# Optimization experiments

Measured on AMD Instinct MI355X. Metric: run time of the kernel, lower is better.

## Reference

```python
import jax, jax.numpy as jnp
import numpy as np

N, F, H, O, D = 4096, 128, 4, 64, 64


def setup_inputs() -> dict:
    key = jax.random.key(0)
    k1, k2, k3, k4, k5 = jax.random.split(key, 5)
    h = jax.random.normal(k1, (1, N, F), dtype=jnp.float32)
    # dense binary adjacency (0/1)
    a = jax.random.randint(k2, (1, N, N), 0, 2).astype(jnp.float32)
    kernel = jax.random.normal(k3, (H, F, O), dtype=jnp.float32) * 0.1
    attn_kernel = jax.random.normal(k4, (H, F, D), dtype=jnp.float32) * 0.1
    attn_kernel2 = jax.random.normal(k5, (H, F, D), dtype=jnp.float32) * 0.1
    return {"h": h, "a": a, "kernel": kernel, "attn_kernel": attn_kernel, "attn_kernel2": attn_kernel2}


def reference(h, a, kernel, attn_kernel, attn_kernel2):
    x = h[0]          # [N, F]
    adj = a[0]        # [N, N] dense 0/1 adjacency
    # per-head linear projections, vectorized over heads
    feats = jnp.einsum('nf,hfo->hno', x, kernel)          # [H, N, O]
    f_self = jnp.einsum('nf,hfd->hnd', x, attn_kernel)    # [H, N, D]
    f_other = jnp.einsum('nf,hfd->hnd', x, attn_kernel2)  # [H, N, D]
    # dense attention logits, masked BEFORE the nonlinearity (as in original)
    dense = jnp.einsum('hnd,hmd->hnm', f_self, f_other)   # [H, N, N]
    masked = adj[None] * dense
    masked = jnp.where(masked >= 0, masked, 0.2 * masked)  # LeakyReLU(0.2)
    masked = masked / jnp.sqrt(jnp.asarray(D, jnp.float32))
    neg_inf = jnp.where(adj == 0, jnp.float32(-1e9), jnp.float32(0.0))  # [N, N]
    att = jax.nn.softmax(masked + neg_inf[None], axis=-1)
    att = att * (adj != 0).astype(att.dtype)[None]
    # aggregation (dropout is identity at inference, rate=0)
    node_features = jnp.einsum('hnm,hmo->hno', att, feats)  # [H, N, O]
    node_features = jax.nn.relu(node_features)
    # zero out padding rows (all-zero input features)
    row_mask = (jnp.sum((x != 0).astype(jnp.float32), axis=-1, keepdims=True) > 0).astype(jnp.float32)  # [N, 1]
    node_features = node_features * row_mask[None]
    # concat heads along last dim -> [1, N, H*O]
    out = jnp.transpose(node_features, (1, 0, 2)).reshape(N, H * O)
    return out[None]
```

## Files before the change

### kernel.cpp

```cpp
#include <hip/hip_runtime.h>
#include <hip/hip_bf16.h>

typedef unsigned short u16;
typedef unsigned int u32;
typedef unsigned long long u64;
typedef __attribute__((ext_vector_type(8))) short bf16x8;
typedef __attribute__((ext_vector_type(4))) float f32x4;
typedef __attribute__((ext_vector_type(4))) u16 u16x4;

#define N 4096
#define F 128
#define H 4
#define O 64
#define NW (N / 64)
#define NT 16
#define QSCALE 0.18033688011112043f

__device__ inline float exp2_hw(float x) {
#if __has_builtin(__builtin_amdgcn_exp2f)
  return __builtin_amdgcn_exp2f(x);
#else
  return __expf(x * 0.6931471805599453f);
#endif
}

__device__ inline u16 f2bf(float f) {
  union { __hip_bfloat16 b; u16 u; } v;
  v.b = __float2bfloat16(f);
  return v.u;
}

__global__ __launch_bounds__(256) void prep_kernel(
    const float* __restrict__ x, const float* __restrict__ adj,
    const float* __restrict__ wv, const float* __restrict__ wq,
    const float* __restrict__ wk, u16* __restrict__ Q, u16* __restrict__ K,
    u16* __restrict__ Vt, float* __restrict__ rmask, u64* __restrict__ bits) {
  const int b = blockIdx.x;
  const int t = threadIdx.x;

  if (b < 1024) {
    const int w = t >> 6, l = t & 63;
    const int row = b * 4 + w;
    const float* ar = adj + (size_t)row * N;
    u64* br = bits + (size_t)row * NW;
#pragma unroll 4
    for (int j2 = 0; j2 < 16; j2++) {
      float4 v = *(const float4*)&ar[j2 * 256 + l * 4];
      unsigned nib = (unsigned)(v.x != 0.f) | ((unsigned)(v.y != 0.f) << 1) |
                     ((unsigned)(v.z != 0.f) << 2) | ((unsigned)(v.w != 0.f) << 3);
      u64 word = (u64)nib << ((l & 15) * 4);
      word |= __shfl_xor(word, 1);
      word |= __shfl_xor(word, 2);
      word |= __shfl_xor(word, 4);
      word |= __shfl_xor(word, 8);
      if ((l & 15) == 0) br[j2 * 4 + (l >> 4)] = word;
    }
  } else if (b < 1792) {
    __shared__ float xs[64][132];
    __shared__ float wsh[128][64];
    const int pb = b - 1024;
    const int brow = (pb & 63) * 64;
    const int p = pb >> 6, h = p / 3, which = p % 3;
    const float* W = (which == 0 ? wq : which == 1 ? wk : wv) + h * F * O;

#pragma unroll
    for (int i = 0; i < 8; i++) {
      int idx = t + i * 256, r = idx >> 5, c4 = idx & 31;
      *(float4*)&xs[r][c4 * 4] = *(const float4*)&x[(brow + r) * F + c4 * 4];
    }
#pragma unroll
    for (int i = 0; i < 8; i++) {
      int idx = t + i * 256, r = idx >> 4, c4 = idx & 15;
      *(float4*)&wsh[r][c4 * 4] = *(const float4*)&W[r * O + c4 * 4];
    }
    __syncthreads();

    const int r0 = (t >> 4) << 2, c0 = (t & 15) << 2;
    float acc[4][4] = {};
#pragma unroll 8
    for (int f = 0; f < F; f++) {
      float4 bb = *(float4*)&wsh[f][c0];
      float a0 = xs[r0 + 0][f], a1 = xs[r0 + 1][f];
      float a2 = xs[r0 + 2][f], a3 = xs[r0 + 3][f];
      acc[0][0] = fmaf(a0, bb.x, acc[0][0]); acc[0][1] = fmaf(a0, bb.y, acc[0][1]);
      acc[0][2] = fmaf(a0, bb.z, acc[0][2]); acc[0][3] = fmaf(a0, bb.w, acc[0][3]);
      acc[1][0] = fmaf(a1, bb.x, acc[1][0]); acc[1][1] = fmaf(a1, bb.y, acc[1][1]);
      acc[1][2] = fmaf(a1, bb.z, acc[1][2]); acc[1][3] = fmaf(a1, bb.w, acc[1][3]);
      acc[2][0] = fmaf(a2, bb.x, acc[2][0]); acc[2][1] = fmaf(a2, bb.y, acc[2][1]);
      acc[2][2] = fmaf(a2, bb.z, acc[2][2]); acc[2][3] = fmaf(a2, bb.w, acc[2][3]);
      acc[3][0] = fmaf(a3, bb.x, acc[3][0]); acc[3][1] = fmaf(a3, bb.y, acc[3][1]);
      acc[3][2] = fmaf(a3, bb.z, acc[3][2]); acc[3][3] = fmaf(a3, bb.w, acc[3][3]);
    }

    if (which == 0) {
      u16* dst = Q + h * N * O;
#pragma unroll
      for (int i = 0; i < 4; i++) {
        u16x4 v4 = { f2bf(acc[i][0] * QSCALE), f2bf(acc[i][1] * QSCALE),
                     f2bf(acc[i][2] * QSCALE), f2bf(acc[i][3] * QSCALE) };
        *(u16x4*)&dst[(brow + r0 + i) * O + c0] = v4;
      }
    } else if (which == 1) {
      u16* dst = K + h * N * O;
#pragma unroll
      for (int i = 0; i < 4; i++) {
        u16x4 v4 = { f2bf(acc[i][0]), f2bf(acc[i][1]), f2bf(acc[i][2]), f2bf(acc[i][3]) };
        *(u16x4*)&dst[(brow + r0 + i) * O + c0] = v4;
      }
    } else {
      u16* dst = Vt + h * O * N;
#pragma unroll
      for (int j = 0; j < 4; j++) {
        u16x4 v4 = { f2bf(acc[0][j]), f2bf(acc[1][j]), f2bf(acc[2][j]), f2bf(acc[3][j]) };
        *(u16x4*)&dst[(c0 + j) * N + brow + r0] = v4;
      }
    }
  } else {
    int n = (b - 1792) * 256 + t;
    const float4* xr = (const float4*)(x + n * F);
    float s = 0.f;
#pragma unroll
    for (int i = 0; i < F / 4; i++) {
      float4 v = xr[i];
      s += fabsf(v.x) + fabsf(v.y) + fabsf(v.z) + fabsf(v.w);
    }
    rmask[n] = (s != 0.f) ? 1.f : 0.f;
  }
}

__global__ __launch_bounds__(512) void attn_kernel(
    const u64* __restrict__ bits, const u16* __restrict__ Qg,
    const u16* __restrict__ Kg, const u16* __restrict__ Vtg,
    float* __restrict__ Opart, float* __restrict__ Spart) {
  __shared__ __align__(16) char kv[2][4][8192];
  __shared__ __align__(16) u16 pst[8][16][64];

  const int tid = threadIdx.x;
  const int w = tid >> 6, l = tid & 63;
  const int lm = l & 15, lg = l >> 4;
  const int rg = w >> 1, hc = w & 1;
  const int h = blockIdx.y;
  const int z = blockIdx.z;
  const int R0 = blockIdx.x * 64;
  const int WR0 = R0 + rg * 16;
  const int CB0 = z * 2048;

  const char* Kb = (const char*)(Kg + h * N * O);
  const char* Vb = (const char*)(Vtg + h * O * N);
  const u64* bblk = bits + (size_t)WR0 * NW;

  const int srow = w * 8 + (l >> 3);
  const int scol = ((l & 7) * 16) ^ ((srow & 7) << 4);

  const u16* Qh = Qg + h * N * O;
  bf16x8 qa0 = *(const bf16x8*)&Qh[(WR0 + lm) * O + lg * 8];
  bf16x8 qa1 = *(const bf16x8*)&Qh[(WR0 + lm) * O + 32 + lg * 8];

  bf16x8 ones;
#pragma unroll
  for (int i = 0; i < 8; i++) ones[i] = (short)0x3F80;

  char* pbase = (char*)&pst[w][0][0];
  const char* prd0 = pbase + lm * 128 + ((lg * 16) ^ ((lm & 7) << 4));
  const char* prd1 = pbase + lm * 128 + ((64 + lg * 16) ^ ((lm & 7) << 4));

  f32x4 oacc[4];
  f32x4 lacc = {0.f, 0.f, 0.f, 0.f};
#pragma unroll
  for (int i = 0; i < 4; i++) oacc[i] = (f32x4){0.f, 0.f, 0.f, 0.f};
  const f32x4 zero4 = {0.f, 0.f, 0.f, 0.f};

  auto STAGE = [&](int b, int t) {
    __builtin_amdgcn_global_load_lds(
        (const u32*)(Kb + (size_t)(CB0 + 0 * 1024 + t * 64 + srow) * 128 + scol),
        (u32*)&kv[b][0][w * 1024], 16, 0, 0);
    __builtin_amdgcn_global_load_lds(
        (const u32*)(Kb + (size_t)(CB0 + 1 * 1024 + t * 64 + srow) * 128 + scol),
        (u32*)&kv[b][1][w * 1024], 16, 0, 0);
    __builtin_amdgcn_global_load_lds(
        (const u32*)(Vb + (size_t)srow * (N * 2) + (CB0 + 0 * 1024 + t * 64) * 2 + scol),
        (u32*)&kv[b][2][w * 1024], 16, 0, 0);
    __builtin_amdgcn_global_load_lds(
        (const u32*)(Vb + (size_t)srow * (N * 2) + (CB0 + 1 * 1024 + t * 64) * 2 + scol),
        (u32*)&kv[b][3][w * 1024], 16, 0, 0);
  };

  STAGE(0, 0);
  __syncthreads();

  int b = 0;
#pragma unroll 1
  for (int t = 0; t < NT; ++t) {
    if (t + 1 < NT) STAGE(b ^ 1, t + 1);

    const int widx = (CB0 >> 6) + hc * NT + t;

    u64 sh0 = bblk[(lg * 4 + 0) * NW + widx] >> lm;
    u64 sh1 = bblk[(lg * 4 + 1) * NW + widx] >> lm;
    u64 sh2 = bblk[(lg * 4 + 2) * NW + widx] >> lm;
    u64 sh3 = bblk[(lg * 4 + 3) * NW + widx] >> lm;

    const char* Kt = &kv[b][hc][0];
    f32x4 sacc[4];
    __builtin_amdgcn_s_setprio(1);
#pragma unroll
    for (int tt = 0; tt < 4; tt++) {
      const int row = tt * 16 + lm;
      const int sw = (row & 7) << 4;
      bf16x8 kb0 = *(const bf16x8*)(Kt + row * 128 + ((lg * 16) ^ sw));
      bf16x8 kb1 = *(const bf16x8*)(Kt + row * 128 + ((lg * 16 + 64) ^ sw));
      f32x4 s0 = __builtin_amdgcn_mfma_f32_16x16x32_bf16(qa0, kb0, zero4, 0, 0, 0);
      sacc[tt] = __builtin_amdgcn_mfma_f32_16x16x32_bf16(qa1, kb1, s0, 0, 0, 0);
    }
    __builtin_amdgcn_s_setprio(0);

#pragma unroll
    for (int tt = 0; tt < 4; tt++) {
#pragma unroll
      for (int r = 0; r < 4; r++) {
        u64 sh = (r == 0 ? sh0 : r == 1 ? sh1 : r == 2 ? sh2 : sh3);
        unsigned bit = (unsigned)(sh >> (tt * 16)) & 1u;
        float sv = sacc[tt][r];
        float lv = fmaxf(sv, 0.2f * sv);
        float p = bit ? exp2_hw(lv) : 0.f;
        const int prow = lg * 4 + r;
        *(u16*)(pbase + prow * 128 +
                ((((tt * 16 + lm) * 2)) ^ ((prow & 7) << 4))) = f2bf(p);
      }
    }
    bf16x8 pa0 = *(const bf16x8*)prd0;
    bf16x8 pa1 = *(const bf16x8*)prd1;

    const char* Vt_ = &kv[b][2 + hc][0];
    __builtin_amdgcn_s_setprio(1);
#pragma unroll
    for (int ot = 0; ot < 4; ot++) {
      const int o = ot * 16 + lm;
      const int sw = (o & 7) << 4;
      bf16x8 vb0 = *(const bf16x8*)(Vt_ + o * 128 + ((lg * 16) ^ sw));
      bf16x8 vb1 = *(const bf16x8*)(Vt_ + o * 128 + ((lg * 16 + 64) ^ sw));
      oacc[ot] = __builtin_amdgcn_mfma_f32_16x16x32_bf16(pa0, vb0, oacc[ot], 0, 0, 0);
      oacc[ot] = __builtin_amdgcn_mfma_f32_16x16x32_bf16(pa1, vb1, oacc[ot], 0, 0, 0);
    }
    lacc = __builtin_amdgcn_mfma_f32_16x16x32_bf16(pa0, ones, lacc, 0, 0, 0);
    lacc = __builtin_amdgcn_mfma_f32_16x16x32_bf16(pa1, ones, lacc, 0, 0, 0);
    __builtin_amdgcn_s_setprio(0);

    __syncthreads();
    b ^= 1;
  }

  float (*Om2)[64][64] = (float (*)[64][64])&kv[0][0][0];
#pragma unroll
  for (int ot = 0; ot < 4; ot++)
#pragma unroll
    for (int r = 0; r < 4; r++)
      Om2[hc][rg * 16 + lg * 4 + r][ot * 16 + lm] = oacc[ot][r];
  if (lm == 0) {
    float* ps = (float*)pbase;
#pragma unroll
    for (int r = 0; r < 4; r++) ps[lg * 4 + r] = lacc[r];
  }
  __syncthreads();

  const int row = tid >> 3;
  const int c0 = (tid & 7) * 8;
  const int grow = R0 + row;
  float* op = &Opart[(((size_t)z * H + h) * N + grow) * O + c0];
#pragma unroll
  for (int j = 0; j < 8; j++)
    op[j] = Om2[0][row][c0 + j] + Om2[1][row][c0 + j];
  if ((tid & 7) == 0) {
    const int rg2 = row >> 4, ri = row & 15;
    float s0 = ((float*)&pst[rg2 * 2 + 0][0][0])[ri];
    float s1 = ((float*)&pst[rg2 * 2 + 1][0][0])[ri];
    Spart[((size_t)z * H + h) * N + grow] = s0 + s1;
  }
}

__global__ __launch_bounds__(256) void merge_kernel(
    const float* __restrict__ Opart, const float* __restrict__ Spart,
    const float* __restrict__ rowmask, float* __restrict__ out) {
  const int h = blockIdx.y;
  const int idx = blockIdx.x * 256 + threadIdx.x;
  const int row = idx >> 4, c0 = (idx & 15) * 4;
  float S = Spart[(size_t)h * N + row] + Spart[((size_t)H + h) * N + row];
  float inv = (S > 0.f) ? 1.f / S : 0.f;
  float rm = rowmask[row];
  const float4 o0 = *(const float4*)&Opart[((size_t)h * N + row) * O + c0];
  const float4 o1 = *(const float4*)&Opart[(((size_t)H + h) * N + row) * O + c0];
  float4 r;
  r.x = fmaxf((o0.x + o1.x) * inv, 0.f) * rm;
  r.y = fmaxf((o0.y + o1.y) * inv, 0.f) * rm;
  r.z = fmaxf((o0.z + o1.z) * inv, 0.f) * rm;
  r.w = fmaxf((o0.w + o1.w) * inv, 0.f) * rm;
  *(float4*)&out[(size_t)row * (H * O) + h * O + c0] = r;
}

extern "C" void kernel_launch(void* const* d_in, const int* in_sizes, int n_in,
                              void* d_out, int out_size, void* d_ws, size_t ws_size,
                              hipStream_t stream) {
  const float* x   = (const float*)d_in[0];
  const float* adj = (const float*)d_in[1];
  const float* wv  = (const float*)d_in[2];
  const float* wq  = (const float*)d_in[3];
  const float* wk  = (const float*)d_in[4];
  float* out = (float*)d_out;

  u16* Q  = (u16*)d_ws;
  u16* K  = Q + H * N * O;
  u16* Vt = K + H * N * O;
  float* rmask = (float*)(Vt + H * N * O);
  u64* bits = (u64*)(rmask + N);
  float* Opart = (float*)(bits + (size_t)N * NW);
  float* Spart = Opart + (size_t)2 * H * N * O;

  prep_kernel<<<dim3(1808), 256, 0, stream>>>(x, adj, wv, wq, wk, Q, K, Vt, rmask, bits);
  attn_kernel<<<dim3(N / 64, H, 2), 512, 0, stream>>>(bits, Q, K, Vt, Opart, Spart);
  merge_kernel<<<dim3(N * O / 4 / 256, H), 256, 0, stream>>>(Opart, Spart, rmask, out);
}
```

Before: 75.69 us.

## Overlap next-tile K/V loads with compute using explicit vmcnt waits and barriers

Replaces the per-iteration __syncthreads with a manual s_waitcnt vmcnt(8) plus raw s_barrier. The next tile's global_load_lds transfers can then stay in flight while the current tile's MFMA and softmax work runs, instead of being drained at every iteration end. The adjacency bitmask words are also prefetched one iteration ahead into registers, so their latency no longer sits on the critical path. The cost is that correctness now depends on exact counting of outstanding vector-memory operations and on sched_barrier placement.

```diff
diff --git a/kernel.cpp b/kernel.cpp
--- a/kernel.cpp
+++ b/kernel.cpp
@@ -185,20 +185,29 @@
         (u32*)&kv[b][3][w * 1024], 16, 0, 0);
   };
 
+  const int wb = (CB0 >> 6) + hc * NT;
+  u64 cur0 = bblk[(lg * 4 + 0) * NW + wb];
+  u64 cur1 = bblk[(lg * 4 + 1) * NW + wb];
+  u64 cur2 = bblk[(lg * 4 + 2) * NW + wb];
+  u64 cur3 = bblk[(lg * 4 + 3) * NW + wb];
   STAGE(0, 0);
-  __syncthreads();
 
   int b = 0;
 #pragma unroll 1
   for (int t = 0; t < NT; ++t) {
-    if (t + 1 < NT) STAGE(b ^ 1, t + 1);
-
-    const int widx = (CB0 >> 6) + hc * NT + t;
-
-    u64 sh0 = bblk[(lg * 4 + 0) * NW + widx] >> lm;
-    u64 sh1 = bblk[(lg * 4 + 1) * NW + widx] >> lm;
-    u64 sh2 = bblk[(lg * 4 + 2) * NW + widx] >> lm;
-    u64 sh3 = bblk[(lg * 4 + 3) * NW + widx] >> lm;
+    u64 nx0 = 0, nx1 = 0, nx2 = 0, nx3 = 0;
+    if (t + 1 < NT) {
+      nx0 = bblk[(lg * 4 + 0) * NW + wb + t + 1];
+      nx1 = bblk[(lg * 4 + 1) * NW + wb + t + 1];
+      nx2 = bblk[(lg * 4 + 2) * NW + wb + t + 1];
+      nx3 = bblk[(lg * 4 + 3) * NW + wb + t + 1];
+      STAGE(b ^ 1, t + 1);
+      asm volatile("s_waitcnt vmcnt(8)" ::: "memory");
+    } else {
+      asm volatile("s_waitcnt vmcnt(0)" ::: "memory");
+    }
+    __builtin_amdgcn_s_barrier();
+    __builtin_amdgcn_sched_barrier(0);
 
     const char* Kt = &kv[b][hc][0];
     f32x4 sacc[4];
@@ -218,8 +227,8 @@
     for (int tt = 0; tt < 4; tt++) {
 #pragma unroll
       for (int r = 0; r < 4; r++) {
-        u64 sh = (r == 0 ? sh0 : r == 1 ? sh1 : r == 2 ? sh2 : sh3);
-        unsigned bit = (unsigned)(sh >> (tt * 16)) & 1u;
+        u64 cr = (r == 0 ? cur0 : r == 1 ? cur1 : r == 2 ? cur2 : cur3);
+        unsigned bit = (unsigned)(cr >> (tt * 16 + lm)) & 1u;
         float sv = sacc[tt][r];
         float lv = fmaxf(sv, 0.2f * sv);
         float p = bit ? exp2_hw(lv) : 0.f;
@@ -246,7 +255,9 @@
     lacc = __builtin_amdgcn_mfma_f32_16x16x32_bf16(pa1, ones, lacc, 0, 0, 0);
     __builtin_amdgcn_s_setprio(0);
 
-    __syncthreads();
+    __builtin_amdgcn_sched_barrier(0);
+    __builtin_amdgcn_s_barrier();
+    cur0 = nx0; cur1 = nx1; cur2 = nx2; cur3 = nx3;
     b ^= 1;
   }
 
```

Result: no change. 76.13 us (+0.6%).
